# Performance work log

Hardware: AMD Instinct MI355X
Metric: run time of the kernel (lower is better)

## Reference

```python
import jax, jax.numpy as jnp
import numpy as np

N = 100_000
E = 1_600_000
IN_DIM = 21
HID = 256
OUT = 256


def setup_inputs() -> dict:
    key = jax.random.key(0)
    ks = jax.random.split(key, 10)
    node_scalar = jax.random.normal(ks[0], (N, IN_DIM), dtype=jnp.float32)
    edge_index = jax.random.randint(ks[1], (2, E), 0, N, dtype=jnp.int64)
    s_in = 1.0 / np.sqrt(IN_DIM)
    s_h = 1.0 / np.sqrt(HID)
    W_in = jax.random.uniform(ks[2], (IN_DIM, HID), jnp.float32, -s_in, s_in)
    b_in = jax.random.uniform(ks[3], (HID,), jnp.float32, -s_in, s_in)
    W_self = jax.random.uniform(ks[4], (HID, HID), jnp.float32, -s_h, s_h)
    b_self = jax.random.uniform(ks[5], (HID,), jnp.float32, -s_h, s_h)
    W_nei = jax.random.uniform(ks[6], (HID, HID), jnp.float32, -s_h, s_h)
    b_nei = jax.random.uniform(ks[7], (HID,), jnp.float32, -s_h, s_h)
    W_out = jax.random.uniform(ks[8], (HID, OUT), jnp.float32, -s_h, s_h)
    b_out = jax.random.uniform(ks[9], (OUT,), jnp.float32, -s_h, s_h)
    return {
        "node_scalar": node_scalar,
        "W_in": W_in, "b_in": b_in,
        "W_self": W_self, "b_self": b_self,
        "W_nei": W_nei, "b_nei": b_nei,
        "W_out": W_out, "b_out": b_out,
        "edge_index": edge_index,
    }


def reference(node_scalar, W_in, b_in, W_self, b_self, W_nei, b_nei, W_out, b_out, edge_index):
    # x = relu(Linear(node_scalar)); dropout is identity in eval mode
    x = jax.nn.relu(node_scalar @ W_in + b_in)           # (N, H)
    n = x.shape[0]
    src, dst = edge_index[0], edge_index[1]
    msg = x[src]                                          # (E, H) gather
    agg = jax.ops.segment_sum(msg, dst, num_segments=n)   # (N, H) scatter-add
    deg = jax.ops.segment_sum(jnp.ones((dst.shape[0],), dtype=x.dtype), dst, num_segments=n)
    agg = agg / jnp.maximum(deg, 1.0)[:, None]            # degree mean (clamp_min 1)
    h = jax.nn.relu(x @ W_self + b_self + agg @ W_nei + b_nei)
    g = h.mean(axis=0)                                    # global mean pool -> (H,)
    return g @ W_out + b_out                              # (OUT,)
```

## Files before the change

### kernel.cpp

```cpp
#include <hip/hip_runtime.h>
#include <hip/hip_bf16.h>

#define HID 256
#define IND 21
#define PB 6400
#define MAXB 512

typedef short short8 __attribute__((ext_vector_type(8)));
typedef float floatx16 __attribute__((ext_vector_type(16)));
typedef float floatx2 __attribute__((ext_vector_type(2)));

__device__ inline unsigned short f2bf(float f) {
  __hip_bfloat16 h = __float2bfloat16(f);
  union { __hip_bfloat16 h; unsigned short u; } c;
  c.h = h;
  return c.u;
}

__device__ inline unsigned int pk_bf16_trunc(floatx2 p) {
  union { float f; unsigned int u; } a, b;
  a.f = p.x; b.f = p.y;
  return (b.u & 0xffff0000u) | (a.u >> 16);
}

__device__ inline void acc8p(uint2 v, floatx2* a) {
  a[0] += __builtin_amdgcn_cvt_pk_f32_fp8((int)v.x, false);
  a[1] += __builtin_amdgcn_cvt_pk_f32_fp8((int)v.x, true);
  a[2] += __builtin_amdgcn_cvt_pk_f32_fp8((int)v.y, false);
  a[3] += __builtin_amdgcn_cvt_pk_f32_fp8((int)v.y, true);
}

__device__ inline short8 mk_s8(unsigned a, unsigned b, unsigned c, unsigned d) {
  union { uint4 u; short8 s; } x; x.u = make_uint4(a, b, c, d); return x.s;
}

__device__ inline short8 dec8(uint2 v) {
  unsigned w0 = pk_bf16_trunc(__builtin_amdgcn_cvt_pk_f32_fp8((int)v.x, false));
  unsigned w1 = pk_bf16_trunc(__builtin_amdgcn_cvt_pk_f32_fp8((int)v.x, true));
  unsigned w2 = pk_bf16_trunc(__builtin_amdgcn_cvt_pk_f32_fp8((int)v.y, false));
  unsigned w3 = pk_bf16_trunc(__builtin_amdgcn_cvt_pk_f32_fp8((int)v.y, true));
  return mk_s8(w0, w1, w2, w3);
}

__device__ inline void gl16(const unsigned char* g, unsigned char* l) {
  __builtin_amdgcn_global_load_lds(
      (const __attribute__((address_space(1))) unsigned char*)g,
      (__attribute__((address_space(3))) unsigned char*)l, 16, 0, 0);
}

__global__ __launch_bounds__(256) void k_front(
    const float* __restrict__ ns, const float* __restrict__ Win,
    const float* __restrict__ bin, uint2* __restrict__ xq2,
    uint2* __restrict__ Aqx,
    const float* __restrict__ Wself, const float* __restrict__ Wnei,
    unsigned short* __restrict__ Bf16,
    const int* __restrict__ dst, int* __restrict__ bcnt,
    int N, int E, int nb2, int G1) {
  int blk = blockIdx.x;
  int tid = threadIdx.x;
  if (blk < G1) {
    __shared__ float s[8][IND];
    __shared__ float fx[8][257];
    int nb = blk * 8;
    if (tid < 8 * IND) {
      int idx = nb * IND + tid;
      s[tid / IND][tid % IND] = (idx < N * IND) ? ns[idx] : 0.f;
    }
    float w[IND];
#pragma unroll
    for (int k = 0; k < IND; k++) w[k] = Win[k * HID + tid];
    float b = bin[tid];
    __syncthreads();
#pragma unroll
    for (int j = 0; j < 8; j++) {
      float acc = b;
#pragma unroll
      for (int k = 0; k < IND; k++) acc += s[j][k] * w[k];
      fx[j][tid] = acc > 0.f ? acc : 0.f;
    }
    __syncthreads();
    {
      int j = tid & 7, u = tid >> 3;
      int node = nb + j;
      if (node < N) {
        const float* fp = &fx[j][u * 8];
        int lo0 = __builtin_amdgcn_cvt_pk_fp8_f32(fp[0], fp[1], 0, false);
        int w0  = __builtin_amdgcn_cvt_pk_fp8_f32(fp[2], fp[3], lo0, true);
        int lo1 = __builtin_amdgcn_cvt_pk_fp8_f32(fp[4], fp[5], 0, false);
        int w1  = __builtin_amdgcn_cvt_pk_fp8_f32(fp[6], fp[7], lo1, true);
        uint2 val = make_uint2((unsigned)w0, (unsigned)w1);
        xq2[(size_t)node * 32 + u] = val;
        int g = node >> 5, row = node & 31, c = u >> 1, hi = u & 1;
        Aqx[(size_t)(g * 16 + c) * 64 + hi * 32 + row] = val;
      }
    }
  } else if (blk < G1 + 256) {
    int n = blk - G1;
    int ct = n >> 5, l5 = n & 31;
#pragma unroll
    for (int t = 0; t < 2; t++) {
      int k = tid + t * 256;
      float v = (k < HID) ? Wself[k * HID + n] : Wnei[(k - HID) * HID + n];
      int c = k >> 4, kin = k & 15;
      int lane = (kin >> 3) * 32 + l5;
      int j = kin & 7;
      Bf16[(size_t)((c * 8 + ct) * 64 + lane) * 8 + j] = f2bf(v);
    }
  } else {
    __shared__ int lh[MAXB];
    int e0 = (blk - G1 - 256) * PB;
    for (int b = tid; b < nb2; b += 256) lh[b] = 0;
    __syncthreads();
    int c = min(PB, E - e0);
    for (int i = tid; i < c; i += 256) atomicAdd(&lh[dst[e0 + i] >> 8], 1);
    __syncthreads();
    for (int b = tid; b < nb2; b += 256)
      if (lh[b]) atomicAdd(&bcnt[b], lh[b]);
  }
}

__global__ __launch_bounds__(512) void k_bscan(
    const int* __restrict__ bcnt, int* __restrict__ bbase, int* __restrict__ bcur,
    int* __restrict__ row_start, int E, int N, int nb2) {
  __shared__ int ts[512];
  int tid = threadIdx.x;
  int v = (tid < nb2) ? bcnt[tid] : 0;
  ts[tid] = v;
  __syncthreads();
  for (int off = 1; off < 512; off <<= 1) {
    int t = (tid >= off) ? ts[tid - off] : 0;
    __syncthreads();
    ts[tid] += t;
    __syncthreads();
  }
  if (tid < nb2) { bbase[tid] = ts[tid] - v; bcur[tid] = ts[tid] - v; }
  if (tid == 0) { bbase[nb2] = E; row_start[N] = E; }
}

__global__ __launch_bounds__(256) void k_part(
    const int* __restrict__ src, const int* __restrict__ dst,
    int* __restrict__ bcur, unsigned int* __restrict__ ebuf, int E, int nb2) {
  __shared__ int lh[MAXB];
  int tid = threadIdx.x;
  int e0 = blockIdx.x * PB;
  for (int b = tid; b < nb2; b += 256) lh[b] = 0;
  __syncthreads();
  int cnt = min(PB, E - e0);
  for (int i = tid; i < cnt; i += 256) atomicAdd(&lh[dst[e0 + i] >> 8], 1);
  __syncthreads();
  for (int b = tid; b < nb2; b += 256) {
    int c = lh[b];
    lh[b] = (c > 0) ? atomicAdd(&bcur[b], c) : 0;
  }
  __syncthreads();
  for (int i = tid; i < cnt; i += 256) {
    int s = src[e0 + i];
    int d = dst[e0 + i];
    int pos = atomicAdd(&lh[d >> 8], 1);
    ebuf[pos] = ((unsigned)s << 8) | ((unsigned)d & 255u);
  }
}

__global__ __launch_bounds__(256) void k_fill2(
    const unsigned int* __restrict__ ebuf, const int* __restrict__ bbase,
    int* __restrict__ row_start, unsigned int* __restrict__ csr, int N) {
  __shared__ int lcnt[256];
  __shared__ int lcur[256];
  __shared__ int ts[256];
  int b = blockIdx.x;
  int tid = threadIdx.x;
  int start = bbase[b], end = bbase[b + 1];
  lcnt[tid] = 0;
  __syncthreads();
  for (int i = start + tid; i < end; i += 256)
    atomicAdd(&lcnt[ebuf[i] & 255u], 1);
  __syncthreads();
  int v = lcnt[tid];
  ts[tid] = v;
  __syncthreads();
  for (int off = 1; off < 256; off <<= 1) {
    int t = (tid >= off) ? ts[tid - off] : 0;
    __syncthreads();
    ts[tid] += t;
    __syncthreads();
  }
  int excl = start + ts[tid] - v;
  int node = (b << 8) + tid;
  if (node < N) row_start[node] = excl;
  lcur[tid] = excl;
  __syncthreads();
  for (int i = start + tid; i < end; i += 256) {
    unsigned int e = ebuf[i];
    int pos = atomicAdd(&lcur[e & 255u], 1);
    csr[pos] = e & ~255u;
  }
}

__global__ __launch_bounds__(256) void k_agg(
    const unsigned char* __restrict__ xqb, const unsigned int* __restrict__ csrb,
    const int* __restrict__ row_start, uint2* __restrict__ aggrm, int N) {
  int wid = (int)((blockIdx.x * (unsigned)blockDim.x + threadIdx.x) >> 6);
  int lane = threadIdx.x & 63;
  int half = lane >> 5;
  int l32 = lane & 31;
  if (wid >= N) return;
  int start = row_start[wid];
  int end = row_start[wid + 1];
  int c = end - start;
  unsigned lo = (unsigned)(l32 * 8);
  floatx2 a[4], b[4], d[4], e[4];
#pragma unroll
  for (int j = 0; j < 4; j++) {
    a[j] = (floatx2){0.f, 0.f}; b[j] = (floatx2){0.f, 0.f};
    d[j] = (floatx2){0.f, 0.f}; e[j] = (floatx2){0.f, 0.f};
  }
  int i = 0;
  for (; i + 8 <= c; i += 8) {
    unsigned o0 = csrb[start + i + half] + lo;
    unsigned o1 = csrb[start + i + 2 + half] + lo;
    unsigned o2 = csrb[start + i + 4 + half] + lo;
    unsigned o3 = csrb[start + i + 6 + half] + lo;
    uint2 v0 = *(const uint2*)(xqb + o0);
    uint2 v1 = *(const uint2*)(xqb + o1);
    uint2 v2 = *(const uint2*)(xqb + o2);
    uint2 v3 = *(const uint2*)(xqb + o3);
    acc8p(v0, a); acc8p(v1, b); acc8p(v2, d); acc8p(v3, e);
  }
  for (; i + 2 <= c; i += 2) {
    unsigned o0 = csrb[start + i + half] + lo;
    uint2 v0 = *(const uint2*)(xqb + o0);
    acc8p(v0, a);
  }
  if ((c & 1) && half == 0) {
    unsigned o0 = csrb[start + c - 1] + lo;
    uint2 v0 = *(const uint2*)(xqb + o0);
    acc8p(v0, a);
  }
#pragma unroll
  for (int j = 0; j < 4; j++) a[j] += b[j] + d[j] + e[j];

  float f[8];
#pragma unroll
  for (int j = 0; j < 4; j++) { f[2 * j] = a[j].x; f[2 * j + 1] = a[j].y; }
#pragma unroll
  for (int j = 0; j < 8; j++) f[j] += __shfl_xor(f[j], 32);

  if (half == 0) {
    float inv = 1.0f / fmaxf((float)c, 1.0f);
#pragma unroll
    for (int j = 0; j < 8; j++) f[j] *= inv;
    int lo0 = __builtin_amdgcn_cvt_pk_fp8_f32(f[0], f[1], 0, false);
    int w0  = __builtin_amdgcn_cvt_pk_fp8_f32(f[2], f[3], lo0, true);
    int lo1 = __builtin_amdgcn_cvt_pk_fp8_f32(f[4], f[5], 0, false);
    int w1  = __builtin_amdgcn_cvt_pk_fp8_f32(f[6], f[7], lo1, true);
    aggrm[(size_t)wid * 32 + l32] = make_uint2((unsigned)w0, (unsigned)w1);
  }
}

__global__ __launch_bounds__(256) void k_tr(
    const uint2* __restrict__ rm, uint2* __restrict__ fr, int N) {
  __shared__ uint2 ld[64 * 33];
  int b = blockIdx.x;
  int tid = threadIdx.x;
  int n0 = b * 64;
#pragma unroll
  for (int j = 0; j < 8; j++) {
    int idx = j * 256 + tid;
    int nl = idx >> 5, u = idx & 31;
    int node = n0 + nl;
    uint2 v = (node < N) ? rm[(size_t)node * 32 + u] : make_uint2(0u, 0u);
    ld[nl * 33 + u] = v;
  }
  __syncthreads();
  size_t obase = (size_t)b * 2048;
#pragma unroll
  for (int j = 0; j < 8; j++) {
    int oidx = j * 256 + tid;
    int gg = oidx >> 10, rem = oidx & 1023;
    int c = rem >> 6, hr = rem & 63, hi = hr >> 5, row = hr & 31;
    int nl = gg * 32 + row, u = c * 2 + hi;
    fr[obase + oidx] = ld[nl * 33 + u];
  }
}

__global__ __launch_bounds__(256, 3) void k_h(
    const unsigned char* __restrict__ Aqx, const unsigned char* __restrict__ Aqagg,
    const unsigned char* __restrict__ Bf8, const float* __restrict__ bself,
    const float* __restrict__ bnei, float* __restrict__ hpart, int N) {
  __shared__ __align__(16) unsigned char As[2][8192];
  __shared__ __align__(16) unsigned char Bs[2][16384];
  __shared__ float colsum[128];
  int tid = threadIdx.x;
  int lane = tid & 63;
  int w = tid >> 6;
  int wr = w >> 1, wc = w & 1;
  int l32 = lane & 31, half = lane >> 5;
  int bx = blockIdx.x, by = blockIdx.y;
  int rowBase = bx * 128;

  if (tid < 128) colsum[tid] = 0.f;

  floatx16 acc[2][2];
#pragma unroll
  for (int i = 0; i < 2; i++)
#pragma unroll
    for (int j = 0; j < 2; j++) acc[i][j] = (floatx16)(0.f);

  size_t a_grp = (size_t)(bx * 4 + w) * 16 * 512;
  int lb = lane * 16;

  {
    const unsigned char* asrc = Aqx + a_grp + lb;
    gl16(asrc, As[0] + w * 2048);
    gl16(asrc + 1024, As[0] + w * 2048 + 1024);
#pragma unroll
    for (int fi = 0; fi < 4; fi++) {
      int ctg = by * 4 + fi;
      gl16(Bf8 + (size_t)(w * 8 + ctg) * 1024 + lb, Bs[0] + (w * 4 + fi) * 1024);
    }
  }

  for (int ch = 0; ch < 8; ch++) {
    int buf = ch & 1;
    __syncthreads();
    if (ch < 7) {
      int cn = ch + 1;
      const unsigned char* Aq = (cn < 4) ? Aqx : Aqagg;
      const unsigned char* asrc = Aq + a_grp + (size_t)(cn & 3) * 2048 + lb;
      unsigned char* ad = As[buf ^ 1] + w * 2048;
      gl16(asrc, ad);
      gl16(asrc + 1024, ad + 1024);
#pragma unroll
      for (int fi = 0; fi < 4; fi++) {
        int cg = cn * 4 + w;
        int ctg = by * 4 + fi;
        gl16(Bf8 + (size_t)(cg * 8 + ctg) * 1024 + lb,
             Bs[buf ^ 1] + (w * 4 + fi) * 1024);
      }
    }
#pragma unroll
    for (int cl = 0; cl < 4; cl++) {
      short8 afr[2];
#pragma unroll
      for (int rt = 0; rt < 2; rt++) {
        uint2 av = *(const uint2*)&As[buf][(wr * 2 + rt) * 2048 + cl * 512 + lane * 8];
        afr[rt] = dec8(av);
      }
#pragma unroll
      for (int ctw = 0; ctw < 2; ctw++) {
        short8 bfr = *(const short8*)&Bs[buf][(cl * 4 + wc * 2 + ctw) * 1024 + lane * 16];
#pragma unroll
        for (int rt = 0; rt < 2; rt++)
          acc[rt][ctw] = __builtin_amdgcn_mfma_f32_32x32x16_bf16(
              afr[rt], bfr, acc[rt][ctw], 0, 0, 0);
      }
    }
  }

#pragma unroll
  for (int ctw = 0; ctw < 2; ctw++) {
    int lcol = (wc * 2 + ctw) * 32 + l32;
    int gcol = by * 128 + lcol;
    float bb = bself[gcol] + bnei[gcol];
    float psum = 0.f;
#pragma unroll
    for (int rt = 0; rt < 2; rt++) {
#pragma unroll
      for (int r = 0; r < 16; r++) {
        int rw = rowBase + wr * 64 + rt * 32 + (r & 3) + 8 * (r >> 2) + 4 * half;
        float v = acc[rt][ctw][r] + bb;
        v = v > 0.f ? v : 0.f;
        if (rw < N) psum += v;
      }
    }
    atomicAdd(&colsum[lcol], psum);
  }
  __syncthreads();
  if (tid < 128) hpart[(size_t)bx * 256 + by * 128 + tid] = colsum[tid];
}

__global__ __launch_bounds__(256) void k_red(
    const float* __restrict__ hpart, float* __restrict__ gsum, int nbx) {
  int c = threadIdx.x;
  float s = 0.f;
  for (int i = blockIdx.x; i < nbx; i += gridDim.x)
    s += hpart[(size_t)i * 256 + c];
  atomicAdd(&gsum[c], s);
}

__global__ __launch_bounds__(HID) void k_out(
    const float* __restrict__ gsum, const float* __restrict__ Wout,
    const float* __restrict__ bout, float* __restrict__ out, float invN) {
  __shared__ float g[HID];
  int c = threadIdx.x;
  g[c] = gsum[c] * invN;
  __syncthreads();
  float acc = bout[c];
#pragma unroll 8
  for (int k = 0; k < HID; k++) acc += g[k] * Wout[k * HID + c];
  out[c] = acc;
}

extern "C" void kernel_launch(void* const* d_in, const int* in_sizes, int n_in,
                              void* d_out, int out_size, void* d_ws, size_t ws_size,
                              hipStream_t stream) {
  const float* ns    = (const float*)d_in[0];
  const float* Win   = (const float*)d_in[1];
  const float* bin   = (const float*)d_in[2];
  const float* Wself = (const float*)d_in[3];
  const float* bself = (const float*)d_in[4];
  const float* Wnei  = (const float*)d_in[5];
  const float* bnei  = (const float*)d_in[6];
  const float* Wout  = (const float*)d_in[7];
  const float* bout  = (const float*)d_in[8];
  const int*   eidx  = (const int*)d_in[9];

  int N = in_sizes[0] / IND;
  int E = in_sizes[9] / 2;
  const int* src = eidx;
  const int* dst = eidx + E;
  int nb2 = (N + 255) >> 8;
  int nbx = (N + 127) / 128;
  size_t NGU = (size_t)nbx * 4 * 16 * 64;

  unsigned int* xq     = (unsigned int*)d_ws;
  uint2* Aqx           = (uint2*)(xq + (size_t)N * 64);
  uint2* Aqagg         = Aqx + NGU;
  uint2* aggrm         = Aqagg + NGU;
  unsigned short* Bf16 = (unsigned short*)(aggrm + (size_t)N * 32);
  unsigned int* csr  = (unsigned int*)(Bf16 + 256 * 512);
  unsigned int* ebuf = csr + E;
  int* row_start = (int*)(ebuf + E);
  int* bcnt      = row_start + N + 1;
  int* bbase     = bcnt + MAXB;
  int* bcur      = bbase + MAXB + 1;
  float* gsum    = (float*)(bcur + MAXB);
  float* hpart   = gsum + HID;

  hipMemsetAsync(bcnt, 0, MAXB * sizeof(int), stream);
  hipMemsetAsync(gsum, 0, HID * sizeof(float), stream);

  int G1 = (N + 7) / 8;
  int pgrid = (E + PB - 1) / PB;
  k_front<<<G1 + 256 + pgrid, 256, 0, stream>>>(
      ns, Win, bin, (uint2*)xq, Aqx, Wself, Wnei, Bf16, dst, bcnt,
      N, E, nb2, G1);

  k_bscan<<<1, 512, 0, stream>>>(bcnt, bbase, bcur, row_start, E, N, nb2);
  k_part<<<pgrid, 256, 0, stream>>>(src, dst, bcur, ebuf, E, nb2);
  k_fill2<<<nb2, 256, 0, stream>>>(ebuf, bbase, row_start, csr, N);

  int agrid = (N + 3) / 4;
  k_agg<<<agrid, 256, 0, stream>>>((const unsigned char*)xq, csr, row_start,
                                   aggrm, N);

  int tgrid = (N + 63) / 64;
  k_tr<<<tgrid, 256, 0, stream>>>(aggrm, Aqagg, N);

  dim3 hgrid(nbx, 2);
  k_h<<<hgrid, 256, 0, stream>>>((const unsigned char*)Aqx,
                                 (const unsigned char*)Aqagg,
                                 (const unsigned char*)Bf16,
                                 bself, bnei, hpart, N);

  k_red<<<64, 256, 0, stream>>>(hpart, gsum, nbx);
  k_out<<<1, HID, 0, stream>>>(gsum, Wout, bout, (float*)d_out, 1.0f / (float)N);
}
```

Before: 301.2 us.

## Fuse aggregation with fragment transpose and swizzle k_h block order

The aggregation kernel now processes 32 nodes per block, staging the quantized fp8 mean rows in shared memory and writing them straight into the MFMA fragment layout. This removes the separate transpose kernel and the intermediate row-major buffer round-trip. The h-GEMM launch becomes a 1D grid with a remapped block order that groups the two column halves of nearby row tiles, so A tiles are reused while still in cache. Each wave now walks 8 nodes one after another, which may reduce latency hiding in the gather.

```diff
diff --git a/kernel.cpp b/kernel.cpp
--- a/kernel.cpp
+++ b/kernel.cpp
@@ -198,104 +198,102 @@
 
 __global__ __launch_bounds__(256) void k_agg(
     const unsigned char* __restrict__ xqb, const unsigned int* __restrict__ csrb,
-    const int* __restrict__ row_start, uint2* __restrict__ aggrm, int N) {
-  int wid = (int)((blockIdx.x * (unsigned)blockDim.x + threadIdx.x) >> 6);
-  int lane = threadIdx.x & 63;
+    const int* __restrict__ row_start, uint2* __restrict__ Aqagg, int N) {
+  __shared__ uint2 ld[32][33];
+  int tid = threadIdx.x;
+  int lane = tid & 63;
+  int w = tid >> 6;
   int half = lane >> 5;
   int l32 = lane & 31;
-  if (wid >= N) return;
-  int start = row_start[wid];
-  int end = row_start[wid + 1];
-  int c = end - start;
+  int g0 = blockIdx.x * 32;
   unsigned lo = (unsigned)(l32 * 8);
-  floatx2 a[4], b[4], d[4], e[4];
+
+  for (int nl = w * 8; nl < w * 8 + 8; nl++) {
+    int wid = g0 + nl;
+    int cw = (wid < N) ? wid : (N - 1);
+    int start = row_start[cw];
+    int end = row_start[cw + 1];
+    int c = end - start;
+    floatx2 a[4], b[4], d[4], e[4];
+#pragma unroll
+    for (int j = 0; j < 4; j++) {
+      a[j] = (floatx2){0.f, 0.f}; b[j] = (floatx2){0.f, 0.f};
+      d[j] = (floatx2){0.f, 0.f}; e[j] = (floatx2){0.f, 0.f};
+    }
+    int i = 0;
+    for (; i + 8 <= c; i += 8) {
+      unsigned o0 = csrb[start + i + half] + lo;
+      unsigned o1 = csrb[start + i + 2 + half] + lo;
+      unsigned o2 = csrb[start + i + 4 + half] + lo;
+      unsigned o3 = csrb[start + i + 6 + half] + lo;
+      uint2 v0 = *(const uint2*)(xqb + o0);
+      uint2 v1 = *(const uint2*)(xqb + o1);
+      uint2 v2 = *(const uint2*)(xqb + o2);
+      uint2 v3 = *(const uint2*)(xqb + o3);
+      acc8p(v0, a); acc8p(v1, b); acc8p(v2, d); acc8p(v3, e);
+    }
+    for (; i + 2 <= c; i += 2) {
+      unsigned o0 = csrb[start + i + half] + lo;
+      uint2 v0 = *(const uint2*)(xqb + o0);
+      acc8p(v0, a);
+    }
+    if ((c & 1) && half == 0) {
+      unsigned o0 = csrb[start + c - 1] + lo;
+      uint2 v0 = *(const uint2*)(xqb + o0);
+      acc8p(v0, a);
+    }
+#pragma unroll
+    for (int j = 0; j < 4; j++) a[j] += b[j] + d[j] + e[j];
+
+    float f[8];
+#pragma unroll
+    for (int j = 0; j < 4; j++) { f[2 * j] = a[j].x; f[2 * j + 1] = a[j].y; }
+#pragma unroll
+    for (int j = 0; j < 8; j++) f[j] += __shfl_xor(f[j], 32);
+
+    if (half == 0) {
+      float inv = 1.0f / fmaxf((float)c, 1.0f);
+#pragma unroll
+      for (int j = 0; j < 8; j++) f[j] *= inv;
+      int lo0 = __builtin_amdgcn_cvt_pk_fp8_f32(f[0], f[1], 0, false);
+      int w0  = __builtin_amdgcn_cvt_pk_fp8_f32(f[2], f[3], lo0, true);
+      int lo1 = __builtin_amdgcn_cvt_pk_fp8_f32(f[4], f[5], 0, false);
+      int w1  = __builtin_amdgcn_cvt_pk_fp8_f32(f[6], f[7], lo1, true);
+      ld[nl][l32] = make_uint2((unsigned)w0, (unsigned)w1);
+    }
+  }
+  __syncthreads();
+  size_t obase = (size_t)blockIdx.x * 1024;
 #pragma unroll
   for (int j = 0; j < 4; j++) {
-    a[j] = (floatx2){0.f, 0.f}; b[j] = (floatx2){0.f, 0.f};
-    d[j] = (floatx2){0.f, 0.f}; e[j] = (floatx2){0.f, 0.f};
-  }
-  int i = 0;
-  for (; i + 8 <= c; i += 8) {
-    unsigned o0 = csrb[start + i + half] + lo;
-    unsigned o1 = csrb[start + i + 2 + half] + lo;
-    unsigned o2 = csrb[start + i + 4 + half] + lo;
-    unsigned o3 = csrb[start + i + 6 + half] + lo;
-    uint2 v0 = *(const uint2*)(xqb + o0);
-    uint2 v1 = *(const uint2*)(xqb + o1);
-    uint2 v2 = *(const uint2*)(xqb + o2);
-    uint2 v3 = *(const uint2*)(xqb + o3);
-    acc8p(v0, a); acc8p(v1, b); acc8p(v2, d); acc8p(v3, e);
-  }
-  for (; i + 2 <= c; i += 2) {
-    unsigned o0 = csrb[start + i + half] + lo;
-    uint2 v0 = *(const uint2*)(xqb + o0);
-    acc8p(v0, a);
-  }
-  if ((c & 1) && half == 0) {
-    unsigned o0 = csrb[start + c - 1] + lo;
-    uint2 v0 = *(const uint2*)(xqb + o0);
-    acc8p(v0, a);
-  }
-#pragma unroll
-  for (int j = 0; j < 4; j++) a[j] += b[j] + d[j] + e[j];
-
-  float f[8];
-#pragma unroll
-  for (int j = 0; j < 4; j++) { f[2 * j] = a[j].x; f[2 * j + 1] = a[j].y; }
-#pragma unroll
-  for (int j = 0; j < 8; j++) f[j] += __shfl_xor(f[j], 32);
-
-  if (half == 0) {
-    float inv = 1.0f / fmaxf((float)c, 1.0f);
-#pragma unroll
-    for (int j = 0; j < 8; j++) f[j] *= inv;
-    int lo0 = __builtin_amdgcn_cvt_pk_fp8_f32(f[0], f[1], 0, false);
-    int w0  = __builtin_amdgcn_cvt_pk_fp8_f32(f[2], f[3], lo0, true);
-    int lo1 = __builtin_amdgcn_cvt_pk_fp8_f32(f[4], f[5], 0, false);
-    int w1  = __builtin_amdgcn_cvt_pk_fp8_f32(f[6], f[7], lo1, true);
-    aggrm[(size_t)wid * 32 + l32] = make_uint2((unsigned)w0, (unsigned)w1);
-  }
-}
-
-__global__ __launch_bounds__(256) void k_tr(
-    const uint2* __restrict__ rm, uint2* __restrict__ fr, int N) {
-  __shared__ uint2 ld[64 * 33];
-  int b = blockIdx.x;
-  int tid = threadIdx.x;
-  int n0 = b * 64;
-#pragma unroll
-  for (int j = 0; j < 8; j++) {
-    int idx = j * 256 + tid;
-    int nl = idx >> 5, u = idx & 31;
-    int node = n0 + nl;
-    uint2 v = (node < N) ? rm[(size_t)node * 32 + u] : make_uint2(0u, 0u);
-    ld[nl * 33 + u] = v;
-  }
-  __syncthreads();
-  size_t obase = (size_t)b * 2048;
-#pragma unroll
-  for (int j = 0; j < 8; j++) {
     int oidx = j * 256 + tid;
-    int gg = oidx >> 10, rem = oidx & 1023;
-    int c = rem >> 6, hr = rem & 63, hi = hr >> 5, row = hr & 31;
-    int nl = gg * 32 + row, u = c * 2 + hi;
-    fr[obase + oidx] = ld[nl * 33 + u];
+    int cc = oidx >> 6, hr = oidx & 63, hi = hr >> 5, row = hr & 31;
+    Aqagg[obase + oidx] = ld[row][cc * 2 + hi];
   }
 }
 
 __global__ __launch_bounds__(256, 3) void k_h(
     const unsigned char* __restrict__ Aqx, const unsigned char* __restrict__ Aqagg,
     const unsigned char* __restrict__ Bf8, const float* __restrict__ bself,
-    const float* __restrict__ bnei, float* __restrict__ hpart, int N) {
+    const float* __restrict__ bnei, float* __restrict__ hpart, int N, int nfull) {
   __shared__ __align__(16) unsigned char As[2][8192];
   __shared__ __align__(16) unsigned char Bs[2][16384];
   __shared__ float colsum[128];
+  int bid = blockIdx.x;
+  int bx, by;
+  if (bid < nfull) {
+    bx = (bid >> 4) * 8 + (bid & 7);
+    by = (bid >> 3) & 1;
+  } else {
+    int rem = bid - nfull;
+    bx = (nfull >> 1) + (rem >> 1);
+    by = rem & 1;
+  }
   int tid = threadIdx.x;
   int lane = tid & 63;
   int w = tid >> 6;
   int wr = w >> 1, wc = w & 1;
   int l32 = lane & 31, half = lane >> 5;
-  int bx = blockIdx.x, by = blockIdx.y;
   int rowBase = bx * 128;
 
   if (tid < 128) colsum[tid] = 0.f;
@@ -426,8 +424,7 @@
   unsigned int* xq     = (unsigned int*)d_ws;
   uint2* Aqx           = (uint2*)(xq + (size_t)N * 64);
   uint2* Aqagg         = Aqx + NGU;
-  uint2* aggrm         = Aqagg + NGU;
-  unsigned short* Bf16 = (unsigned short*)(aggrm + (size_t)N * 32);
+  unsigned short* Bf16 = (unsigned short*)(Aqagg + NGU);
   unsigned int* csr  = (unsigned int*)(Bf16 + 256 * 512);
   unsigned int* ebuf = csr + E;
   int* row_start = (int*)(ebuf + E);
@@ -450,18 +447,16 @@
   k_part<<<pgrid, 256, 0, stream>>>(src, dst, bcur, ebuf, E, nb2);
   k_fill2<<<nb2, 256, 0, stream>>>(ebuf, bbase, row_start, csr, N);
 
-  int agrid = (N + 3) / 4;
+  int agrid = (N + 31) / 32;
   k_agg<<<agrid, 256, 0, stream>>>((const unsigned char*)xq, csr, row_start,
-                                   aggrm, N);
-
-  int tgrid = (N + 63) / 64;
-  k_tr<<<tgrid, 256, 0, stream>>>(aggrm, Aqagg, N);
-
-  dim3 hgrid(nbx, 2);
-  k_h<<<hgrid, 256, 0, stream>>>((const unsigned char*)Aqx,
-                                 (const unsigned char*)Aqagg,
-                                 (const unsigned char*)Bf16,
-                                 bself, bnei, hpart, N);
+                                   Aqagg, N);
+
+  int nblocks = nbx * 2;
+  int nfull = (nblocks / 16) * 16;
+  k_h<<<nblocks, 256, 0, stream>>>((const unsigned char*)Aqx,
+                                   (const unsigned char*)Aqagg,
+                                   (const unsigned char*)Bf16,
+                                   bself, bnei, hpart, N, nfull);
 
   k_red<<<64, 256, 0, stream>>>(hpart, gsum, nbx);
   k_out<<<1, HID, 0, stream>>>(gsum, Wout, bout, (float*)d_out, 1.0f / (float)N);
```

Measured after the change: 293.4 us. 2.6% less time.
